# Optimization experiments

Hardware: AMD Instinct MI355X
Metric: run time of the kernel (lower is better)

## Reference

```python
import jax, jax.numpy as jnp
import numpy as np

EPS = 1e-4
HEADS = 8
DIM_HEAD = 32
BALANCE = 0.3


def _normalize(x, dims):
    # torch normalize(): norm over `dims` in fp32; norm = eps + norm*sqrt(norm.numel()/x.numel())
    red = 1
    for d in dims:
        red *= x.shape[d]
    norm = jnp.sqrt(jnp.sum(jnp.square(x.astype(jnp.float32)), axis=dims, keepdims=True))
    norm = EPS + norm / np.sqrt(red)
    return x / norm.astype(x.dtype)


def _mpconv1x1(x, w, gain=1.0):
    # MPConv forward (eval mode): weight-normalize per output channel, scale, 1x1 conv
    w = w.astype(jnp.float32)
    w = _normalize(w, (1, 2, 3))
    fan_in = w.shape[1] * w.shape[2] * w.shape[3]
    w = (w * (gain / np.sqrt(fan_in))).astype(x.dtype)[:, :, 0, 0]  # [out, in]
    return jnp.einsum('oi,nihw->nohw', w, x)


def setup_inputs() -> dict:
    key = jax.random.key(0)
    k1, k2, k3 = jax.random.split(key, 3)
    x = jax.random.normal(k1, (2, 256, 48, 48), dtype=jnp.float32)
    w_qkv = jax.random.normal(k2, (768, 256, 1, 1), dtype=jnp.float32)
    w_out = jax.random.normal(k3, (256, 256, 1, 1), dtype=jnp.float32)
    return {"x": x, "w_qkv": w_qkv, "w_out": w_out}


def reference(x, w_qkv, w_out):
    n, c, h, w_sp = x.shape
    seq = h * w_sp
    y = _mpconv1x1(x, w_qkv)                          # [n, 3c, h, w]
    y = y.reshape(n, HEADS, DIM_HEAD, 3, seq)         # channel split: head x dim_head x 3
    y = _normalize(y, (2,))                           # L2-normalize over dim_head axis
    q = y[:, :, :, 0, :]
    k = y[:, :, :, 1, :]
    v = y[:, :, :, 2, :]
    # scores [n, h, q, k] with k scaled by 1/sqrt(dim_head)
    att = jax.nn.softmax(jnp.einsum('nhcq,nhck->nhqk', q, k) / np.sqrt(DIM_HEAD), axis=3)
    y = jnp.einsum('nhqk,nhck->nhcq', att, v)         # [n, heads, dim_head, seq]
    y = _mpconv1x1(y.reshape(n, c, h, w_sp), w_out)
    t = BALANCE
    # mp_sum: lerp then magnitude-preserving rescale
    return (x + t * (y - x)) / np.sqrt((1 - t) ** 2 + t ** 2)
```

## Files before the change

### kernel.cpp

```cpp
#include <hip/hip_runtime.h>
#include <math.h>

#define EPSN 1e-4f
#define SEQ 2304

using bf16x8 = __attribute__((ext_vector_type(8))) short;
using f32x4  = __attribute__((ext_vector_type(4))) float;

__device__ inline unsigned short f2bf(float x) {
    union { float f; unsigned u; } c; c.f = x;
    unsigned u = c.u;
    u += 0x7fffu + ((u >> 16) & 1u);
    return (unsigned short)(u >> 16);
}

__device__ inline unsigned cvt_pk_bf16(float lo, float hi) {
    unsigned r;
    asm("v_cvt_pk_bf16_f32 %0, %1, %2" : "=v"(r) : "v"(lo), "v"(hi));
    return r;
}
__device__ inline void permlane32_swap(unsigned &a, unsigned &b) {
    asm("v_permlane32_swap_b32 %0, %1" : "+v"(a), "+v"(b));
}
__device__ inline void permlane16_swap(unsigned &a, unsigned &b) {
    asm("v_permlane16_swap_b32 %0, %1" : "+v"(a), "+v"(b));
}

__global__ __launch_bounds__(256) void prep_kernel(const float* __restrict__ w_qkv,
                                                   const float* __restrict__ w_out,
                                                   const float* __restrict__ x,
                                                   unsigned short* __restrict__ wqb,
                                                   unsigned short* __restrict__ wob,
                                                   unsigned short* __restrict__ xt) {
    __shared__ __align__(16) unsigned short T[16][72];
    int bid = blockIdx.x;
    if (bid < 256) {
        int wave = threadIdx.x >> 6, lane = threadIdx.x & 63;
        int row = bid * 4 + wave;
        const float* src;
        unsigned short* dst;
        if (row < 768) { src = w_qkv + (size_t)row * 256; dst = wqb + (size_t)row * 256; }
        else           { src = w_out + (size_t)(row - 768) * 256; dst = wob + (size_t)(row - 768) * 256; }
        float4 v = *(const float4*)&src[lane * 4];
        float ss = v.x * v.x + v.y * v.y + v.z * v.z + v.w * v.w;
        for (int off = 32; off > 0; off >>= 1) ss += __shfl_xor(ss, off, 64);
        float sc = 1.0f / (sqrtf(ss) + 16.0f * EPSN);
        unsigned p0 = (unsigned)f2bf(v.x * sc) | ((unsigned)f2bf(v.y * sc) << 16);
        unsigned p1 = (unsigned)f2bf(v.z * sc) | ((unsigned)f2bf(v.w * sc) << 16);
        *(uint2*)&dst[lane * 4] = make_uint2(p0, p1);
    } else {
        int e0 = bid - 256;
        int n = e0 / 576;
        int r = e0 % 576;
        int ct = r / 144;
        int r2 = r % 144;
        int st = r2 >> 2, sq = r2 & 3;
        int tid = threadIdx.x;
        int c = tid >> 2, sv = (tid & 3) * 4;
        float4 v = *(const float4*)&x[(size_t)(n * 256 + ct * 64 + c) * SEQ + st * 64 + sq * 16 + sv];
        T[sv + 0][c] = f2bf(v.x);
        T[sv + 1][c] = f2bf(v.y);
        T[sv + 2][c] = f2bf(v.z);
        T[sv + 3][c] = f2bf(v.w);
        __syncthreads();
        int s = tid >> 4, cb = (tid & 15) * 4;
        uint2 t2 = *(const uint2*)&T[s][cb];
        *(uint2*)&xt[(size_t)(n * SEQ + st * 64 + sq * 16 + s) * 256 + ct * 64 + cb] = t2;
    }
}

__global__ __launch_bounds__(256) void qkv_fused_kernel(const unsigned short* __restrict__ xt,
                                                        const unsigned short* __restrict__ wqb,
                                                        unsigned short* __restrict__ qn,
                                                        unsigned short* __restrict__ kn,
                                                        unsigned short* __restrict__ vn) {
    __shared__ float Cs[96][33];
    __shared__ __align__(16) unsigned short Vls[32][40];
    int bid = blockIdx.x;
    int xcd = bid & 7, j = bid >> 3;
    int h = j & 7;
    int tile = xcd * 18 + (j >> 3);
    int st2 = tile % 72, n = tile / 72;
    int tid = threadIdx.x;
    int wave = tid >> 6, lane = tid & 63;
    int ln = lane & 15, quad = lane >> 4;
    int sgrp = wave & 1, mgrp = wave >> 1;
    const unsigned short* Abase = wqb + (size_t)(h * 96 + mgrp * 48 + ln) * 256 + quad * 8;
    const unsigned short* Bbase = xt + (size_t)(n * SEQ + st2 * 32 + sgrp * 16 + ln) * 256 + quad * 8;
    f32x4 acc[3];
#pragma unroll
    for (int m = 0; m < 3; ++m) acc[m] = (f32x4){0.f, 0.f, 0.f, 0.f};
#pragma unroll
    for (int kc = 0; kc < 8; ++kc) {
        bf16x8 b = *(const bf16x8*)(Bbase + kc * 32);
#pragma unroll
        for (int m = 0; m < 3; ++m) {
            bf16x8 a = *(const bf16x8*)(Abase + (size_t)(m * 16) * 256 + kc * 32);
            acc[m] = __builtin_amdgcn_mfma_f32_16x16x32_bf16(a, b, acc[m], 0, 0, 0);
        }
    }
#pragma unroll
    for (int m = 0; m < 3; ++m)
#pragma unroll
        for (int r = 0; r < 4; ++r)
            Cs[mgrp * 48 + m * 16 + quad * 4 + r][sgrp * 16 + ln] = acc[m][r];
    __syncthreads();
    int nh = n * 8 + h;
    if (tid < 96) {
        int sl = tid & 31, wh = tid >> 5;
        int s = st2 * 32 + sl;
        float v[32];
        float ss = 0.f;
#pragma unroll
        for (int d = 0; d < 32; ++d) { v[d] = Cs[3 * d + wh][sl]; ss += v[d] * v[d]; }
        float inv = 1.0f / (EPSN + sqrtf(ss * (1.0f / 32.0f)));
        if (wh == 0) inv *= 0.17677669529663687f * 1.4426950408889634f;
        if (wh == 2) {
#pragma unroll
            for (int d = 0; d < 32; ++d) Vls[d][sl] = f2bf(v[d] * inv);
        } else {
            unsigned short* dst = (wh == 1 ? kn : qn) + (size_t)nh * 73728 + (size_t)s * 32;
            unsigned wbuf[16];
#pragma unroll
            for (int j2 = 0; j2 < 16; ++j2)
                wbuf[j2] = (unsigned)f2bf(v[2 * j2] * inv) | ((unsigned)f2bf(v[2 * j2 + 1] * inv) << 16);
#pragma unroll
            for (int j2 = 0; j2 < 4; ++j2) {
                uint4 t4 = make_uint4(wbuf[4 * j2], wbuf[4 * j2 + 1], wbuf[4 * j2 + 2], wbuf[4 * j2 + 3]);
                *(uint4*)(dst + j2 * 8) = t4;
            }
        }
    }
    __syncthreads();
    {
        int d = tid >> 3, sj = (tid & 7) * 4;
        uint2 t2 = *(const uint2*)&Vls[d][sj];
        *(uint2*)&vn[(size_t)nh * 73728 + (size_t)d * SEQ + st2 * 32 + sj] = t2;
    }
}

__global__ __launch_bounds__(256) void attn_mfma_kernel(const unsigned short* __restrict__ qn,
                                                        const unsigned short* __restrict__ kn,
                                                        const unsigned short* __restrict__ vn,
                                                        float* __restrict__ Opart,
                                                        float* __restrict__ Lpart) {
    __shared__ __align__(16) unsigned short Ks[2][64][40];
    __shared__ __align__(16) unsigned short Vs[2][32][72];
    int tid = threadIdx.x;
    int wq = tid >> 6, lane = tid & 63;
    int ln = lane & 15, quad = lane >> 4;
    int bid = blockIdx.x;
    int xcd = bid & 7, bi = bid >> 3;
    int nh = xcd * 2 + (bi >= 144);
    int bi2 = (bi >= 144) ? bi - 144 : bi;
    int qt = bi2 % 36, kz = bi2 / 36;
    const unsigned short* Qg = qn + (size_t)nh * 73728;
    const unsigned short* Kg = kn + (size_t)nh * 73728;
    const unsigned short* Vg = vn + (size_t)nh * 73728;

    bf16x8 qf = *(const bf16x8*)(Qg + (size_t)(qt * 64 + wq * 16 + ln) * 32 + quad * 8);
    bf16x8 ones;
#pragma unroll
    for (int i = 0; i < 8; ++i) ones[i] = (short)0x3F80;

    f32x4 o0 = {0.f, 0.f, 0.f, 0.f};
    f32x4 o1 = {0.f, 0.f, 0.f, 0.f};
    f32x4 lac = {0.f, 0.f, 0.f, 0.f};

    const int NT = 9;
    int s0 = kz * NT * 64;

    auto compute_tile = [&](int bsel) {
        const f32x4 zero = {0.f, 0.f, 0.f, 0.f};
        unsigned w[4][2];
#pragma unroll
        for (int c = 0; c < 4; ++c) {
            bf16x8 kf = *(const bf16x8*)(&Ks[bsel][c * 16 + ln][quad * 8]);
            f32x4 sc = __builtin_amdgcn_mfma_f32_16x16x32_bf16(kf, qf, zero, 0, 0, 0);
            w[c][0] = cvt_pk_bf16(exp2f(sc[0]), exp2f(sc[1]));
            w[c][1] = cvt_pk_bf16(exp2f(sc[2]), exp2f(sc[3]));
        }
#pragma unroll
        for (int kc = 0; kc < 2; ++kc) {
            unsigned a0 = w[2 * kc][0], b0 = w[2 * kc + 1][0];
            permlane32_swap(a0, b0);
            permlane16_swap(a0, b0);
            unsigned a1 = w[2 * kc][1], b1 = w[2 * kc + 1][1];
            permlane32_swap(a1, b1);
            permlane16_swap(a1, b1);
            union { unsigned u[4]; bf16x8 v8; } pk;
            pk.u[0] = a0; pk.u[1] = a1; pk.u[2] = b0; pk.u[3] = b1;
            bf16x8 v0 = *(const bf16x8*)(&Vs[bsel][ln][kc * 32 + quad * 8]);
            bf16x8 v1 = *(const bf16x8*)(&Vs[bsel][16 + ln][kc * 32 + quad * 8]);
            lac = __builtin_amdgcn_mfma_f32_16x16x32_bf16(pk.v8, ones, lac, 0, 0, 0);
            o0  = __builtin_amdgcn_mfma_f32_16x16x32_bf16(pk.v8, v0, o0, 0, 0, 0);
            o1  = __builtin_amdgcn_mfma_f32_16x16x32_bf16(pk.v8, v1, o1, 0, 0, 0);
        }
    };

    uint4 kA = *(const uint4*)(Kg + (size_t)s0 * 32 + tid * 8);
    uint4 vA = *(const uint4*)(Vg + (size_t)(tid >> 3) * SEQ + s0 + (tid & 7) * 8);
    *(uint4*)(&Ks[0][tid >> 2][(tid & 3) * 8]) = kA;
    *(uint4*)(&Vs[0][tid >> 3][(tid & 7) * 8]) = vA;
    uint4 kB = *(const uint4*)(Kg + (size_t)(s0 + 64) * 32 + tid * 8);
    uint4 vB = *(const uint4*)(Vg + (size_t)(tid >> 3) * SEQ + (s0 + 64) + (tid & 7) * 8);

    for (int i = 0; i < NT; i += 2) {
        if (i + 2 < NT) {
            int sn = s0 + (i + 2) * 64;
            kA = *(const uint4*)(Kg + (size_t)sn * 32 + tid * 8);
            vA = *(const uint4*)(Vg + (size_t)(tid >> 3) * SEQ + sn + (tid & 7) * 8);
        }
        __syncthreads();
        compute_tile(0);
        if (i + 1 < NT) {
            *(uint4*)(&Ks[1][tid >> 2][(tid & 3) * 8]) = kB;
            *(uint4*)(&Vs[1][tid >> 3][(tid & 7) * 8]) = vB;
        }
        if (i + 3 < NT) {
            int sn = s0 + (i + 3) * 64;
            kB = *(const uint4*)(Kg + (size_t)sn * 32 + tid * 8);
            vB = *(const uint4*)(Vg + (size_t)(tid >> 3) * SEQ + sn + (tid & 7) * 8);
        }
        __syncthreads();
        if (i + 1 < NT) compute_tile(1);
        if (i + 2 < NT) {
            *(uint4*)(&Ks[0][tid >> 2][(tid & 3) * 8]) = kA;
            *(uint4*)(&Vs[0][tid >> 3][(tid & 7) * 8]) = vA;
        }
    }

    float* Ob = Opart + ((size_t)(kz * 16 + nh) * 36 + qt) * 2048;
    float* Lb = Lpart + ((size_t)(kz * 16 + nh) * 36 + qt) * 64;
#pragma unroll
    for (int r = 0; r < 4; ++r) {
        int ql = wq * 16 + quad * 4 + r;
        Ob[ql * 32 + ln]      = o0[r];
        Ob[ql * 32 + 16 + ln] = o1[r];
        if (ln == 0) Lb[ql] = lac[r];
    }
}

__global__ __launch_bounds__(256) void attn_reduce_kernel(const float* __restrict__ Opart,
                                                          const float* __restrict__ Lpart,
                                                          unsigned short* __restrict__ y2t) {
    int qt = blockIdx.x, nh = blockIdx.y;
    int n = nh >> 3, h = nh & 7;
    size_t s0 = (size_t)nh * 36 + qt;
    const float* O0 = Opart + s0 * 2048;
    const float* O1 = Opart + (s0 + 1 * 576) * 2048;
    const float* O2 = Opart + (s0 + 2 * 576) * 2048;
    const float* O3 = Opart + (s0 + 3 * 576) * 2048;
    const float* L0 = Lpart + s0 * 64;
    const float* L1 = Lpart + (s0 + 1 * 576) * 64;
    const float* L2 = Lpart + (s0 + 2 * 576) * 64;
    const float* L3 = Lpart + (s0 + 3 * 576) * 64;
#pragma unroll
    for (int p = 0; p < 2; ++p) {
        int idx = (threadIdx.x + p * 256) * 4;
        int q = idx >> 5, c = idx & 31;
        float inv = 1.0f / (L0[q] + L1[q] + L2[q] + L3[q]);
        float4 a = *(const float4*)&O0[idx];
        float4 b = *(const float4*)&O1[idx];
        float4 e = *(const float4*)&O2[idx];
        float4 f = *(const float4*)&O3[idx];
        float r0 = ((a.x + b.x) + (e.x + f.x)) * inv;
        float r1 = ((a.y + b.y) + (e.y + f.y)) * inv;
        float r2 = ((a.z + b.z) + (e.z + f.z)) * inv;
        float r3 = ((a.w + b.w) + (e.w + f.w)) * inv;
        *(uint2*)&y2t[((size_t)(n * SEQ) + qt * 64 + q) * 256 + h * 32 + c] =
            make_uint2(cvt_pk_bf16(r0, r1), cvt_pk_bf16(r2, r3));
    }
}

__global__ __launch_bounds__(256) void out_gemm_kernel(const unsigned short* __restrict__ y2t,
                                                       const unsigned short* __restrict__ wob,
                                                       const float* __restrict__ x,
                                                       float* __restrict__ out) {
    int bid = blockIdx.x;
    int xcd = bid & 7, j = bid >> 3;
    int mt = j & 3;
    int u = j >> 2;
    int n = u & 1;
    int st = xcd * 18 + (u >> 1);
    int tid = threadIdx.x;
    int wave = tid >> 6, lane = tid & 63;
    int ln = lane & 15, quad = lane >> 4;
    int m0 = mt * 64 + wave * 16;
    const unsigned short* Abase = wob + (size_t)(m0 + ln) * 256 + quad * 8;
    const unsigned short* Bbase = y2t + (size_t)(n * SEQ + st * 16 + ln) * 256 + quad * 8;
    f32x4 acc = (f32x4){0.f, 0.f, 0.f, 0.f};
#pragma unroll
    for (int kc = 0; kc < 8; ++kc) {
        bf16x8 a = *(const bf16x8*)(Abase + kc * 32);
        bf16x8 b = *(const bf16x8*)(Bbase + kc * 32);
        acc = __builtin_amdgcn_mfma_f32_16x16x32_bf16(a, b, acc, 0, 0, 0);
    }
    const float c0f = 0.7f * 1.3130643285972254f;
    const float c1f = 0.3f * 1.3130643285972254f;
#pragma unroll
    for (int r = 0; r < 4; ++r) {
        int o = m0 + quad * 4 + r;
        int s = st * 16 + ln;
        size_t idx = (size_t)(n * 256 + o) * SEQ + s;
        out[idx] = c0f * x[idx] + c1f * acc[r];
    }
}

extern "C" void kernel_launch(void* const* d_in, const int* in_sizes, int n_in,
                              void* d_out, int out_size, void* d_ws, size_t ws_size,
                              hipStream_t stream) {
    (void)in_sizes; (void)n_in; (void)out_size; (void)ws_size;
    const float* x     = (const float*)d_in[0];
    const float* w_qkv = (const float*)d_in[1];
    const float* w_out = (const float*)d_in[2];
    float* out = (float*)d_out;
    float* ws  = (float*)d_ws;
    unsigned short* wqb = (unsigned short*)(ws);
    unsigned short* wob = (unsigned short*)(ws + 98304);
    unsigned short* xt  = (unsigned short*)(ws + 131072);
    unsigned short* y2t = (unsigned short*)(ws + 131072);
    unsigned short* qn  = (unsigned short*)(ws + 720896);
    unsigned short* kn  = (unsigned short*)(ws + 1310720);
    unsigned short* vn  = (unsigned short*)(ws + 1900544);
    float* Opart = ws + 2490368;
    float* Lpart = ws + 7208960;

    hipLaunchKernelGGL(prep_kernel, dim3(1408), dim3(256), 0, stream,
                       w_qkv, w_out, x, wqb, wob, xt);
    hipLaunchKernelGGL(qkv_fused_kernel, dim3(1152), dim3(256), 0, stream,
                       xt, wqb, qn, kn, vn);
    hipLaunchKernelGGL(attn_mfma_kernel, dim3(2304), dim3(256), 0, stream,
                       qn, kn, vn, Opart, Lpart);
    hipLaunchKernelGGL(attn_reduce_kernel, dim3(36, 16), dim3(256), 0, stream,
                       Opart, Lpart, y2t);
    hipLaunchKernelGGL(out_gemm_kernel, dim3(1152), dim3(256), 0, stream,
                       y2t, wob, x, out);
}
```

Baseline: 129.9 us.

## Fuse x transpose into QKV GEMM and split-K reduce into output GEMM

The bf16 transpose of x moves from the prep kernel into the QKV kernel, which now loads fp32 x straight into shared memory. The split-K attention reduction kernel is removed, and the output GEMM now sums the four partial O/L buffers itself and stages them in LDS. This cuts two kernel launches and the xt/y2t intermediate round trips through global memory. In exchange, each QKV block re-reads and converts a 32x256 x tile once per head (8x redundant), and each output block redoes the reduction for all four m-tiles (4x redundant Opart reads).

```diff
diff --git a/kernel.cpp b/kernel.cpp
--- a/kernel.cpp
+++ b/kernel.cpp
@@ -26,54 +26,31 @@
     asm("v_permlane16_swap_b32 %0, %1" : "+v"(a), "+v"(b));
 }
 
-__global__ __launch_bounds__(256) void prep_kernel(const float* __restrict__ w_qkv,
-                                                   const float* __restrict__ w_out,
-                                                   const float* __restrict__ x,
-                                                   unsigned short* __restrict__ wqb,
-                                                   unsigned short* __restrict__ wob,
-                                                   unsigned short* __restrict__ xt) {
-    __shared__ __align__(16) unsigned short T[16][72];
-    int bid = blockIdx.x;
-    if (bid < 256) {
-        int wave = threadIdx.x >> 6, lane = threadIdx.x & 63;
-        int row = bid * 4 + wave;
-        const float* src;
-        unsigned short* dst;
-        if (row < 768) { src = w_qkv + (size_t)row * 256; dst = wqb + (size_t)row * 256; }
-        else           { src = w_out + (size_t)(row - 768) * 256; dst = wob + (size_t)(row - 768) * 256; }
-        float4 v = *(const float4*)&src[lane * 4];
-        float ss = v.x * v.x + v.y * v.y + v.z * v.z + v.w * v.w;
-        for (int off = 32; off > 0; off >>= 1) ss += __shfl_xor(ss, off, 64);
-        float sc = 1.0f / (sqrtf(ss) + 16.0f * EPSN);
-        unsigned p0 = (unsigned)f2bf(v.x * sc) | ((unsigned)f2bf(v.y * sc) << 16);
-        unsigned p1 = (unsigned)f2bf(v.z * sc) | ((unsigned)f2bf(v.w * sc) << 16);
-        *(uint2*)&dst[lane * 4] = make_uint2(p0, p1);
-    } else {
-        int e0 = bid - 256;
-        int n = e0 / 576;
-        int r = e0 % 576;
-        int ct = r / 144;
-        int r2 = r % 144;
-        int st = r2 >> 2, sq = r2 & 3;
-        int tid = threadIdx.x;
-        int c = tid >> 2, sv = (tid & 3) * 4;
-        float4 v = *(const float4*)&x[(size_t)(n * 256 + ct * 64 + c) * SEQ + st * 64 + sq * 16 + sv];
-        T[sv + 0][c] = f2bf(v.x);
-        T[sv + 1][c] = f2bf(v.y);
-        T[sv + 2][c] = f2bf(v.z);
-        T[sv + 3][c] = f2bf(v.w);
-        __syncthreads();
-        int s = tid >> 4, cb = (tid & 15) * 4;
-        uint2 t2 = *(const uint2*)&T[s][cb];
-        *(uint2*)&xt[(size_t)(n * SEQ + st * 64 + sq * 16 + s) * 256 + ct * 64 + cb] = t2;
-    }
-}
-
-__global__ __launch_bounds__(256) void qkv_fused_kernel(const unsigned short* __restrict__ xt,
+__global__ __launch_bounds__(256) void prep_w_kernel(const float* __restrict__ w_qkv,
+                                                     const float* __restrict__ w_out,
+                                                     unsigned short* __restrict__ wqb,
+                                                     unsigned short* __restrict__ wob) {
+    int wave = threadIdx.x >> 6, lane = threadIdx.x & 63;
+    int row = blockIdx.x * 4 + wave;
+    const float* src;
+    unsigned short* dst;
+    if (row < 768) { src = w_qkv + (size_t)row * 256; dst = wqb + (size_t)row * 256; }
+    else           { src = w_out + (size_t)(row - 768) * 256; dst = wob + (size_t)(row - 768) * 256; }
+    float4 v = *(const float4*)&src[lane * 4];
+    float ss = v.x * v.x + v.y * v.y + v.z * v.z + v.w * v.w;
+    for (int off = 32; off > 0; off >>= 1) ss += __shfl_xor(ss, off, 64);
+    float sc = 1.0f / (sqrtf(ss) + 16.0f * EPSN);
+    unsigned p0 = (unsigned)f2bf(v.x * sc) | ((unsigned)f2bf(v.y * sc) << 16);
+    unsigned p1 = (unsigned)f2bf(v.z * sc) | ((unsigned)f2bf(v.w * sc) << 16);
+    *(uint2*)&dst[lane * 4] = make_uint2(p0, p1);
+}
+
+__global__ __launch_bounds__(256) void qkv_fused_kernel(const float* __restrict__ x,
                                                         const unsigned short* __restrict__ wqb,
                                                         unsigned short* __restrict__ qn,
                                                         unsigned short* __restrict__ kn,
                                                         unsigned short* __restrict__ vn) {
+    __shared__ __align__(16) unsigned short Xs[32][264];
     __shared__ float Cs[96][33];
     __shared__ __align__(16) unsigned short Vls[32][40];
     int bid = blockIdx.x;
@@ -85,14 +62,29 @@
     int wave = tid >> 6, lane = tid & 63;
     int ln = lane & 15, quad = lane >> 4;
     int sgrp = wave & 1, mgrp = wave >> 1;
+    int s0 = st2 * 32;
+
+    {
+        int ci = tid >> 3, sv = (tid & 7) * 4;
+#pragma unroll
+        for (int p = 0; p < 8; ++p) {
+            int c = p * 32 + ci;
+            float4 v = *(const float4*)&x[(size_t)(n * 256 + c) * SEQ + s0 + sv];
+            Xs[sv + 0][c] = f2bf(v.x);
+            Xs[sv + 1][c] = f2bf(v.y);
+            Xs[sv + 2][c] = f2bf(v.z);
+            Xs[sv + 3][c] = f2bf(v.w);
+        }
+    }
+    __syncthreads();
+
     const unsigned short* Abase = wqb + (size_t)(h * 96 + mgrp * 48 + ln) * 256 + quad * 8;
-    const unsigned short* Bbase = xt + (size_t)(n * SEQ + st2 * 32 + sgrp * 16 + ln) * 256 + quad * 8;
     f32x4 acc[3];
 #pragma unroll
     for (int m = 0; m < 3; ++m) acc[m] = (f32x4){0.f, 0.f, 0.f, 0.f};
 #pragma unroll
     for (int kc = 0; kc < 8; ++kc) {
-        bf16x8 b = *(const bf16x8*)(Bbase + kc * 32);
+        bf16x8 b = *(const bf16x8*)&Xs[sgrp * 16 + ln][kc * 32 + quad * 8];
 #pragma unroll
         for (int m = 0; m < 3; ++m) {
             bf16x8 a = *(const bf16x8*)(Abase + (size_t)(m * 16) * 256 + kc * 32);
@@ -241,59 +233,58 @@
     }
 }
 
-__global__ __launch_bounds__(256) void attn_reduce_kernel(const float* __restrict__ Opart,
-                                                          const float* __restrict__ Lpart,
-                                                          unsigned short* __restrict__ y2t) {
-    int qt = blockIdx.x, nh = blockIdx.y;
-    int n = nh >> 3, h = nh & 7;
-    size_t s0 = (size_t)nh * 36 + qt;
-    const float* O0 = Opart + s0 * 2048;
-    const float* O1 = Opart + (s0 + 1 * 576) * 2048;
-    const float* O2 = Opart + (s0 + 2 * 576) * 2048;
-    const float* O3 = Opart + (s0 + 3 * 576) * 2048;
-    const float* L0 = Lpart + s0 * 64;
-    const float* L1 = Lpart + (s0 + 1 * 576) * 64;
-    const float* L2 = Lpart + (s0 + 2 * 576) * 64;
-    const float* L3 = Lpart + (s0 + 3 * 576) * 64;
-#pragma unroll
-    for (int p = 0; p < 2; ++p) {
-        int idx = (threadIdx.x + p * 256) * 4;
-        int q = idx >> 5, c = idx & 31;
-        float inv = 1.0f / (L0[q] + L1[q] + L2[q] + L3[q]);
-        float4 a = *(const float4*)&O0[idx];
-        float4 b = *(const float4*)&O1[idx];
-        float4 e = *(const float4*)&O2[idx];
-        float4 f = *(const float4*)&O3[idx];
-        float r0 = ((a.x + b.x) + (e.x + f.x)) * inv;
-        float r1 = ((a.y + b.y) + (e.y + f.y)) * inv;
-        float r2 = ((a.z + b.z) + (e.z + f.z)) * inv;
-        float r3 = ((a.w + b.w) + (e.w + f.w)) * inv;
-        *(uint2*)&y2t[((size_t)(n * SEQ) + qt * 64 + q) * 256 + h * 32 + c] =
-            make_uint2(cvt_pk_bf16(r0, r1), cvt_pk_bf16(r2, r3));
-    }
-}
-
-__global__ __launch_bounds__(256) void out_gemm_kernel(const unsigned short* __restrict__ y2t,
+__global__ __launch_bounds__(256) void out_gemm_kernel(const float* __restrict__ Opart,
+                                                       const float* __restrict__ Lpart,
                                                        const unsigned short* __restrict__ wob,
                                                        const float* __restrict__ x,
                                                        float* __restrict__ out) {
+    __shared__ float Linv[8][16];
+    __shared__ __align__(16) unsigned short Ys[16][264];
     int bid = blockIdx.x;
     int xcd = bid & 7, j = bid >> 3;
     int mt = j & 3;
     int u = j >> 2;
     int n = u & 1;
     int st = xcd * 18 + (u >> 1);
+    int qt = st >> 2;
+    int qo = (st & 3) * 16;
     int tid = threadIdx.x;
+
+    if (tid < 128) {
+        int h = tid >> 4, qi = tid & 15;
+        size_t base = ((size_t)((n * 8 + h) * 36) + qt) * 64 + qo + qi;
+        const size_t kzs = (size_t)16 * 36 * 64;
+        float l = Lpart[base] + Lpart[base + kzs] + Lpart[base + 2 * kzs] + Lpart[base + 3 * kzs];
+        Linv[h][qi] = 1.0f / l;
+    }
+    __syncthreads();
+    {
+        int qi = tid >> 4, dp = tid & 15, d0 = dp * 2;
+        const size_t kzs = (size_t)16 * 36 * 2048;
+#pragma unroll
+        for (int h = 0; h < 8; ++h) {
+            size_t ob = ((size_t)((n * 8 + h) * 36) + qt) * 2048 + (size_t)(qo + qi) * 32 + d0;
+            float2 a = *(const float2*)&Opart[ob];
+            float2 b = *(const float2*)&Opart[ob + kzs];
+            float2 e = *(const float2*)&Opart[ob + 2 * kzs];
+            float2 f = *(const float2*)&Opart[ob + 3 * kzs];
+            float li = Linv[h][qi];
+            float r0 = ((a.x + b.x) + (e.x + f.x)) * li;
+            float r1 = ((a.y + b.y) + (e.y + f.y)) * li;
+            *(unsigned*)&Ys[qi][h * 32 + d0] = cvt_pk_bf16(r0, r1);
+        }
+    }
+    __syncthreads();
+
     int wave = tid >> 6, lane = tid & 63;
     int ln = lane & 15, quad = lane >> 4;
     int m0 = mt * 64 + wave * 16;
     const unsigned short* Abase = wob + (size_t)(m0 + ln) * 256 + quad * 8;
-    const unsigned short* Bbase = y2t + (size_t)(n * SEQ + st * 16 + ln) * 256 + quad * 8;
     f32x4 acc = (f32x4){0.f, 0.f, 0.f, 0.f};
 #pragma unroll
     for (int kc = 0; kc < 8; ++kc) {
         bf16x8 a = *(const bf16x8*)(Abase + kc * 32);
-        bf16x8 b = *(const bf16x8*)(Bbase + kc * 32);
+        bf16x8 b = *(const bf16x8*)&Ys[ln][kc * 32 + quad * 8];
         acc = __builtin_amdgcn_mfma_f32_16x16x32_bf16(a, b, acc, 0, 0, 0);
     }
     const float c0f = 0.7f * 1.3130643285972254f;
@@ -318,22 +309,18 @@
     float* ws  = (float*)d_ws;
     unsigned short* wqb = (unsigned short*)(ws);
     unsigned short* wob = (unsigned short*)(ws + 98304);
-    unsigned short* xt  = (unsigned short*)(ws + 131072);
-    unsigned short* y2t = (unsigned short*)(ws + 131072);
-    unsigned short* qn  = (unsigned short*)(ws + 720896);
-    unsigned short* kn  = (unsigned short*)(ws + 1310720);
-    unsigned short* vn  = (unsigned short*)(ws + 1900544);
-    float* Opart = ws + 2490368;
-    float* Lpart = ws + 7208960;
-
-    hipLaunchKernelGGL(prep_kernel, dim3(1408), dim3(256), 0, stream,
-                       w_qkv, w_out, x, wqb, wob, xt);
+    unsigned short* qn  = (unsigned short*)(ws + 131072);
+    unsigned short* kn  = (unsigned short*)(ws + 720896);
+    unsigned short* vn  = (unsigned short*)(ws + 1310720);
+    float* Opart = ws + 1900544;
+    float* Lpart = ws + 6619136;
+
+    hipLaunchKernelGGL(prep_w_kernel, dim3(256), dim3(256), 0, stream,
+                       w_qkv, w_out, wqb, wob);
     hipLaunchKernelGGL(qkv_fused_kernel, dim3(1152), dim3(256), 0, stream,
-                       xt, wqb, qn, kn, vn);
+                       x, wqb, qn, kn, vn);
     hipLaunchKernelGGL(attn_mfma_kernel, dim3(2304), dim3(256), 0, stream,
                        qn, kn, vn, Opart, Lpart);
-    hipLaunchKernelGGL(attn_reduce_kernel, dim3(36, 16), dim3(256), 0, stream,
-                       Opart, Lpart, y2t);
     hipLaunchKernelGGL(out_gemm_kernel, dim3(1152), dim3(256), 0, stream,
-                       y2t, wob, x, out);
-}
+                       Opart, Lpart, wob, x, out);
+}
```

Result: faster. 123.3 us (-5.1%).
